# Kernel tuning notes

Hardware: AMD Instinct MI355X
Metric: run time of the kernel (lower is better)

The kernel has to match this reference:

```python
import jax, jax.numpy as jnp
import numpy as np

N = 50000   # nodes
E = 800000  # edges (avg degree 16)
F = 128     # feature dim (input = hidden = output)
H = 8       # heads
D = F // H  # head dim = 16
L = 4       # layers


def setup_inputs() -> dict:
    key = jax.random.key(0)
    ks = jax.random.split(key, 11)
    x = jax.random.normal(ks[0], (N, F), dtype=jnp.float32)
    edge_index = jax.random.randint(ks[1], (2, E), 0, N, dtype=jnp.int64)
    s = 1.0 / np.sqrt(F)
    Wq = jax.random.normal(ks[2], (L, F, F), dtype=jnp.float32) * s
    Wk = jax.random.normal(ks[3], (L, F, F), dtype=jnp.float32) * s
    Wv = jax.random.normal(ks[4], (L, F, F), dtype=jnp.float32) * s
    Ws = jax.random.normal(ks[5], (L, F, F), dtype=jnp.float32) * s  # lin_skip (root weight)
    bq = jax.random.normal(ks[6], (L, F), dtype=jnp.float32) * 0.02
    bk = jax.random.normal(ks[7], (L, F), dtype=jnp.float32) * 0.02
    bv = jax.random.normal(ks[8], (L, F), dtype=jnp.float32) * 0.02
    bs = jax.random.normal(ks[9], (L, F), dtype=jnp.float32) * 0.02
    return {"x": x, "edge_index": edge_index, "Wq": Wq, "bq": bq,
            "Wk": Wk, "bk": bk, "Wv": Wv, "bv": bv, "Ws": Ws, "bs": bs}


def _transformer_conv(x, src, dst, Wq, bq, Wk, bk, Wv, bv, Ws, bs):
    # Q from destination nodes, K/V from source nodes (PyG TransformerConv).
    q = (x @ Wq + bq)[dst].reshape(E, H, D)
    k = (x @ Wk + bk)[src].reshape(E, H, D)
    alpha = (q * k).sum(-1) * (1.0 / np.sqrt(D))            # [E, H]
    # segment softmax over edges grouped by destination node
    amax = jax.ops.segment_max(alpha, dst, num_segments=N)   # [N, H]
    amax = jnp.where(jnp.isfinite(amax), amax, 0.0)
    p = jnp.exp(alpha - amax[dst])
    denom = jax.ops.segment_sum(p, dst, num_segments=N)      # [N, H]
    a = p / denom[dst]                                       # [E, H]
    v = (x @ Wv + bv)[src].reshape(E, H, D)
    msg = (a[..., None] * v).reshape(E, F)
    out = jax.ops.segment_sum(msg, dst, num_segments=N)      # concat heads
    out = out + x @ Ws + bs                                  # root/skip connection
    return out, a


def reference(x, edge_index, Wq, bq, Wk, bk, Wv, bv, Ws, bs):
    src, dst = edge_index[0], edge_index[1]
    alphas = []
    h = x
    for i in range(L - 1):
        h, a = _transformer_conv(h, src, dst, Wq[i], bq[i], Wk[i], bk[i],
                                 Wv[i], bv[i], Ws[i], bs[i])
        h = jax.nn.gelu(h, approximate=False)
        alphas.append(a)
    h, a = _transformer_conv(h, src, dst, Wq[-1], bq[-1], Wk[-1], bk[-1],
                             Wv[-1], bv[-1], Ws[-1], bs[-1])
    alphas.append(a)
    return h, jnp.stack(alphas)  # [N, F], [L, E, H]
```

## Files before the change

### kernel.cpp

```cpp
#include <hip/hip_runtime.h>
#include <math.h>

#define F 128
#define HEADS 8

typedef __attribute__((ext_vector_type(8))) short short8;
typedef __attribute__((ext_vector_type(4))) float floatx4;
typedef __attribute__((ext_vector_type(2))) _Float16 half2v;

__device__ __forceinline__ unsigned short f2bf(float f) {
    unsigned u = __float_as_uint(f);
    unsigned r = u + 0x7FFFu + ((u >> 16) & 1u);
    return (unsigned short)(r >> 16);
}

__device__ __forceinline__ half2v ashalf2(unsigned u) {
    return __builtin_bit_cast(half2v, u);
}
__device__ __forceinline__ unsigned pkh(float a, float b) {
    return __builtin_bit_cast(unsigned, __builtin_amdgcn_cvt_pkrtz(a, b));
}

#if __has_builtin(__builtin_amdgcn_fdot2)
#define FDOT2(a, b, c) __builtin_amdgcn_fdot2((a), (b), (c), false)
#else
#define FDOT2(a, b, c) ((c) + (float)(a)[0] * (float)(b)[0] + (float)(a)[1] * (float)(b)[1])
#endif


__global__ __launch_bounds__(256) void setup_k(
    const float* __restrict__ x, unsigned short* __restrict__ xb, int total4,
    const float* __restrict__ Wq, const float* __restrict__ Wk,
    const float* __restrict__ Wv, const float* __restrict__ Ws,
    unsigned short* __restrict__ wfrag, int wtotal,
    int* __restrict__ deg, int* __restrict__ cursor, int N) {
    int idx = blockIdx.x * 256 + threadIdx.x;
    if (idx < total4) {
        float4 v = ((const float4*)x)[idx];
        ushort4 o;
        o.x = f2bf(v.x); o.y = f2bf(v.y); o.z = f2bf(v.z); o.w = f2bf(v.w);
        ((ushort4*)xb)[idx] = o;
        return;
    }
    idx -= total4;
    if (idx < wtotal) {
        int j = idx & 7;
        int lane = (idx >> 3) & 63;
        int rest = idx >> 9;
        int chunk = rest & 3;
        int ftile = (rest >> 2) & 7;
        int mat = (rest >> 5) & 3;
        int layer = rest >> 7;
        int k = chunk * 32 + (lane >> 4) * 8 + j;
        int f = ftile * 16 + (lane & 15);
        const float* W = (mat == 0) ? Wq : (mat == 1) ? Wk : (mat == 2) ? Wv : Ws;
        wfrag[idx] = f2bf(W[((size_t)layer * F + k) * F + f]);
        return;
    }
    idx -= wtotal;
    if (idx < N) deg[idx] = 0;
    else if (idx < 2 * N) cursor[idx - N] = 0;
}


__global__ __launch_bounds__(256) void hist_k(const int* __restrict__ dst, int E, int* __restrict__ deg) {
    int e = blockIdx.x * 256 + threadIdx.x;
    if (e < E) atomicAdd(&deg[dst[e]], 1);
}

__global__ __launch_bounds__(256) void scan1_k(const int* __restrict__ deg, int N,
                                               int* __restrict__ start, int* __restrict__ partials) {
    __shared__ int sm[256];
    int t = threadIdx.x;
    int i = blockIdx.x * 256 + t;
    int v = (i < N) ? deg[i] : 0;
    sm[t] = v;
    __syncthreads();
    for (int off = 1; off < 256; off <<= 1) {
        int add = (t >= off) ? sm[t - off] : 0;
        __syncthreads();
        sm[t] += add;
        __syncthreads();
    }
    if (i < N) start[i] = sm[t] - v;
    if (t == 255) partials[blockIdx.x] = sm[t];
}

__global__ __launch_bounds__(256) void scan23_k(const int* __restrict__ partials, int nb,
                                                int* __restrict__ start, int N, int E) {
    __shared__ int sm[256];
    int t = threadIdx.x;
    int v = (t < nb) ? partials[t] : 0;
    sm[t] = v;
    __syncthreads();
    for (int off = 1; off < 256; off <<= 1) {
        int add = (t >= off) ? sm[t - off] : 0;
        __syncthreads();
        sm[t] += add;
        __syncthreads();
    }
    int myoff = sm[t] - v;
    __syncthreads();
    sm[t] = myoff;
    __syncthreads();
    for (int i = t; i < N; i += 256) start[i] += sm[i >> 8];
    if (t == 0) start[N] = E;
}

__global__ __launch_bounds__(256) void fill_k(const int* __restrict__ src, const int* __restrict__ dst, int E,
                                              const int* __restrict__ start, int* __restrict__ cursor,
                                              int2* __restrict__ epair) {
    int e = blockIdx.x * 256 + threadIdx.x;
    if (e < E) {
        int dd = dst[e];
        int pos = atomicAdd(&cursor[dd], 1);
        epair[start[dd] + pos] = make_int2(e, src[e]);
    }
}


__global__ __launch_bounds__(256) void gemm_mfma(
    const unsigned short* __restrict__ xb, const unsigned short* __restrict__ wfrag,
    const float* __restrict__ bq, const float* __restrict__ bk,
    const float* __restrict__ bv, const float* __restrict__ bs,
    unsigned short* __restrict__ Qh, unsigned short* __restrict__ Kh,
    unsigned short* __restrict__ Vh, unsigned short* __restrict__ Sh, int N) {
    int wave = threadIdx.x >> 6;
    int lane = threadIdx.x & 63;
    int row0 = blockIdx.x * 32;
    int lm = lane & 15, quad = lane >> 4;
    const unsigned short* wf = wfrag + wave * 16384;

    floatx4 acc[2][8];
#pragma unroll
    for (int t = 0; t < 2; t++)
#pragma unroll
        for (int u = 0; u < 8; u++) acc[t][u] = (floatx4){0.f, 0.f, 0.f, 0.f};

#pragma unroll
    for (int chunk = 0; chunk < 4; chunk++) {
        short8 xfr[2];
#pragma unroll
        for (int t = 0; t < 2; t++) {
            int m = row0 + t * 16 + lm;
            m = (m < N) ? m : (N - 1);
            xfr[t] = *(const short8*)(xb + (size_t)m * F + chunk * 32 + quad * 8);
        }
#pragma unroll
        for (int u = 0; u < 8; u++) {
            short8 wfr = *(const short8*)(wf + ((u * 4 + chunk) * 64 + lane) * 8);
            acc[0][u] = __builtin_amdgcn_mfma_f32_16x16x32_bf16(wfr, xfr[0], acc[0][u], 0, 0, 0);
            acc[1][u] = __builtin_amdgcn_mfma_f32_16x16x32_bf16(wfr, xfr[1], acc[1][u], 0, 0, 0);
        }
    }

    const float* bias = (wave == 0) ? bq : (wave == 1) ? bk : (wave == 2) ? bv : bs;
    unsigned short* dp = (wave == 0) ? Qh : (wave == 1) ? Kh : (wave == 2) ? Vh : Sh;
#pragma unroll
    for (int u = 0; u < 8; u++) {
        float4 bv4 = *(const float4*)&bias[u * 16 + quad * 4];
#pragma unroll
        for (int t = 0; t < 2; t++) {
            int node = row0 + t * 16 + lm;
            if (node < N) {
                floatx4 a = acc[t][u];
                size_t off = (size_t)node * F + u * 16 + quad * 4;
                *(uint2*)&dp[off] = make_uint2(pkh(a[0] + bv4.x, a[1] + bv4.y),
                                               pkh(a[2] + bv4.z, a[3] + bv4.w));
            }
        }
    }
}


__device__ __forceinline__ float gelu_exact(float v) {
    return 0.5f * v * (1.0f + erff(v * 0.70710678118654752f));
}

__global__ __launch_bounds__(256) void edge_k(
    const unsigned short* __restrict__ Qh, const unsigned short* __restrict__ Kh,
    const unsigned short* __restrict__ Vh, const unsigned short* __restrict__ Sh,
    const int* __restrict__ start, const int2* __restrict__ epair,
    float* __restrict__ aout,
    float* __restrict__ hout_f, unsigned short* __restrict__ hout_b,
    int N, int do_gelu) {
    __shared__ float wbuf[4][64][8];
    __shared__ int sbuf[4][64];
    __shared__ int ebuf[4][64];
    __shared__ float mdbuf[4][8];

    int wv = threadIdx.x >> 6;
    int lane = threadIdx.x & 63;
    int n = blockIdx.x * 4 + wv;
    if (n >= N) return;

    int beg = start[n], end = start[n + 1];
    int deg = end - beg;
    bool multi = deg > 64;
    int slot = lane >> 3, h = lane & 7;
    int g = lane >> 4, fl = lane & 15;
    int fh = fl >> 1;

    const unsigned short* qp = Qh + (size_t)n * F + h * 16;
    uint4 qa = *(const uint4*)(qp);
    uint4 qc = *(const uint4*)(qp + 8);
    half2v q0 = ashalf2(qa.x), q1 = ashalf2(qa.y), q2 = ashalf2(qa.z), q3 = ashalf2(qa.w);
    half2v q4 = ashalf2(qc.x), q5 = ashalf2(qc.y), q6 = ashalf2(qc.z), q7 = ashalf2(qc.w);

    float d = 0.f;
    float a0 = 0.f, a1 = 0.f, a2 = 0.f, a3 = 0.f, a4 = 0.f, a5 = 0.f, a6 = 0.f, a7 = 0.f;

    for (int c0 = beg; c0 < end; c0 += 64) {
        int cnt = min(64, end - c0);

        int2 pe = epair[c0 + min(lane, cnt - 1)];
        sbuf[wv][lane] = pe.y << 8;
        ebuf[wv][lane] = pe.x;

        int nit = (cnt + 7) >> 3;
        for (int it = 0; it < nit; it++) {
            int idx = it * 8 + slot;
            bool val = idx < cnt;
            int ofs = sbuf[wv][val ? idx : 0];
            const unsigned short* kp = (const unsigned short*)((const char*)Kh + ofs) + h * 16;
            uint4 ka = *(const uint4*)(kp);
            uint4 kc = *(const uint4*)(kp + 8);
            float p0 = 0.f, p1 = 0.f;
            p0 = FDOT2(q0, ashalf2(ka.x), p0);
            p0 = FDOT2(q1, ashalf2(ka.y), p0);
            p0 = FDOT2(q2, ashalf2(ka.z), p0);
            p0 = FDOT2(q3, ashalf2(ka.w), p0);
            p1 = FDOT2(q4, ashalf2(kc.x), p1);
            p1 = FDOT2(q5, ashalf2(kc.y), p1);
            p1 = FDOT2(q6, ashalf2(kc.z), p1);
            p1 = FDOT2(q7, ashalf2(kc.w), p1);
            float w = __expf((p0 + p1) * 0.25f);
            if (!val) w = 0.f;
            d += w;
            wbuf[wv][idx][h] = w;
            if (multi && val) aout[(size_t)ebuf[wv][idx] * HEADS + h] = w;
        }

        for (int j = 0; j < cnt; j += 8) {
            int idx0 = j + g;
            int idx1 = j + 4 + g;
            bool v0 = idx0 < cnt;
            bool v1 = idx1 < cnt;
            int o0s = sbuf[wv][v0 ? idx0 : 0];
            int o1s = sbuf[wv][v1 ? idx1 : 0];
            float w0 = wbuf[wv][v0 ? idx0 : 0][fh];
            float w1 = wbuf[wv][v1 ? idx1 : 0][fh];
            if (!v0) w0 = 0.f;
            if (!v1) w1 = 0.f;
            uint4 va = *(const uint4*)((const char*)Vh + o0s + fl * 16);
            uint4 vb2 = *(const uint4*)((const char*)Vh + o1s + fl * 16);
            half2v x0 = ashalf2(va.x), x1 = ashalf2(va.y), x2 = ashalf2(va.z), x3 = ashalf2(va.w);
            half2v y0 = ashalf2(vb2.x), y1 = ashalf2(vb2.y), y2 = ashalf2(vb2.z), y3 = ashalf2(vb2.w);
            a0 += w0 * (float)x0[0]; a1 += w0 * (float)x0[1];
            a2 += w0 * (float)x1[0]; a3 += w0 * (float)x1[1];
            a4 += w0 * (float)x2[0]; a5 += w0 * (float)x2[1];
            a6 += w0 * (float)x3[0]; a7 += w0 * (float)x3[1];
            a0 += w1 * (float)y0[0]; a1 += w1 * (float)y0[1];
            a2 += w1 * (float)y1[0]; a3 += w1 * (float)y1[1];
            a4 += w1 * (float)y2[0]; a5 += w1 * (float)y2[1];
            a6 += w1 * (float)y3[0]; a7 += w1 * (float)y3[1];
        }
    }

    d += __shfl_xor(d, 8);
    d += __shfl_xor(d, 16);
    d += __shfl_xor(d, 32);
    float inv_d = (d > 0.f) ? 1.f / d : 0.f;
    if (slot == 0) mdbuf[wv][h] = inv_d;

    if (!multi) {
        for (int idx = slot; idx < deg; idx += 8)
            aout[(size_t)ebuf[wv][idx] * HEADS + h] = wbuf[wv][idx][h] * inv_d;
    } else {
        for (int idx = slot; idx < deg; idx += 8)
            aout[(size_t)epair[beg + idx].x * HEADS + h] *= inv_d;
    }

    *(float4*)&wbuf[wv][lane][0] = make_float4(a0, a1, a2, a3);
    *(float4*)&wbuf[wv][lane][4] = make_float4(a4, a5, a6, a7);
    asm volatile("s_waitcnt lgkmcnt(0)" ::: "memory");

    int f0 = lane * 2;
    int frow = f0 >> 3;
    int fcol = f0 & 7;
    float t0 = 0.f, t1 = 0.f;
#pragma unroll
    for (int gg = 0; gg < 4; gg++) {
        float2 pr = *(const float2*)&wbuf[wv][gg * 16 + frow][fcol];
        t0 += pr.x; t1 += pr.y;
    }
    float invd = mdbuf[wv][lane >> 3];
    half2v s2 = ashalf2(*(const unsigned*)&Sh[(size_t)n * F + f0]);
    float o0 = t0 * invd + (float)s2[0];
    float o1 = t1 * invd + (float)s2[1];
    if (do_gelu) {
        o0 = gelu_exact(o0);
        o1 = gelu_exact(o1);
        unsigned ob = (unsigned)f2bf(o0) | ((unsigned)f2bf(o1) << 16);
        *(unsigned*)&hout_b[(size_t)n * F + f0] = ob;
    } else {
        *(float2*)&hout_f[(size_t)n * F + f0] = make_float2(o0, o1);
    }
}


extern "C" void kernel_launch(void* const* d_in, const int* in_sizes, int n_in,
                              void* d_out, int out_size, void* d_ws, size_t ws_size,
                              hipStream_t stream) {
    const float* x  = (const float*)d_in[0];
    const int*   ei = (const int*)d_in[1];
    const float* Wq = (const float*)d_in[2];
    const float* bq = (const float*)d_in[3];
    const float* Wk = (const float*)d_in[4];
    const float* bk = (const float*)d_in[5];
    const float* Wv = (const float*)d_in[6];
    const float* bv = (const float*)d_in[7];
    const float* Ws = (const float*)d_in[8];
    const float* bs = (const float*)d_in[9];

    const int N = in_sizes[0] / F;
    const int E = in_sizes[1] / 2;
    const int L = in_sizes[2] / (F * F);

    unsigned short* Sh = (unsigned short*)d_ws;
    unsigned short* Qh = Sh + (size_t)N * F;
    unsigned short* xb = Qh + (size_t)N * F;
    unsigned short* hb = xb + (size_t)N * F;
    unsigned short* Kb = hb + (size_t)N * F;
    unsigned short* Vb = Kb + (size_t)N * F;
    unsigned short* wfrag = Vb + (size_t)N * F;
    int2* epair = (int2*)(wfrag + (size_t)L * 4 * 16384);
    int* start = (int*)(epair + E);
    int* cursor = start + (N + 1);
    int* deg = cursor + N;
    int* partials = deg + N;

    float* out_h = (float*)d_out;
    float* out_a = out_h + (size_t)N * F;

    const int* srcIdx = ei;
    const int* dstIdx = ei + E;

    int total4 = N * F / 4;
    int wtotal = L * 4 * 16384;
    int stotal = total4 + wtotal + 2 * N;
    setup_k<<<(stotal + 255) / 256, 256, 0, stream>>>(
        x, xb, total4, Wq, Wk, Wv, Ws, wfrag, wtotal, deg, cursor, N);

    int nbScan = (N + 255) / 256;
    hist_k<<<(E + 255) / 256, 256, 0, stream>>>(dstIdx, E, deg);
    scan1_k<<<nbScan, 256, 0, stream>>>(deg, N, start, partials);
    scan23_k<<<1, 256, 0, stream>>>(partials, nbScan, start, N, E);
    fill_k<<<(E + 255) / 256, 256, 0, stream>>>(srcIdx, dstIdx, E, start, cursor, epair);

    for (int l = 0; l < L; ++l) {
        const unsigned short* hin = (l == 0) ? xb : hb;
        gemm_mfma<<<(N + 31) / 32, 256, 0, stream>>>(
            hin, wfrag + (size_t)l * 4 * 16384,
            bq + (size_t)l * F, bk + (size_t)l * F,
            bv + (size_t)l * F, bs + (size_t)l * F,
            Qh, Kb, Vb, Sh, N);
        edge_k<<<(N + 3) / 4, 256, 0, stream>>>(
            Qh, Kb, Vb, Sh, start, epair,
            out_a + (size_t)l * E * HEADS, out_h, hb, N, (l < L - 1) ? 1 : 0);
    }
}
```

Measured before the change: 668.1 us.

## Interleave K and V rows and fuse V aggregation into score loop

The GEMM now writes K and V into one interleaved buffer, 256 halfs per node, so each edge's source row yields K and V from a single 512-byte region. The edge kernel loads V in the same pass as K and accumulates the unnormalized weighted V per head-slot lane, which removes the separate second gather loop over edges. Per-head sums across the eight slots are done with xor shuffles before normalizing and writing through shared memory. This adds 16 accumulators per lane and 48 shuffles, which raises register pressure, and edge work is no longer spread over the lanes the same way.

```diff
diff --git a/kernel.cpp b/kernel.cpp
--- a/kernel.cpp
+++ b/kernel.cpp
@@ -123,8 +123,8 @@
     const unsigned short* __restrict__ xb, const unsigned short* __restrict__ wfrag,
     const float* __restrict__ bq, const float* __restrict__ bk,
     const float* __restrict__ bv, const float* __restrict__ bs,
-    unsigned short* __restrict__ Qh, unsigned short* __restrict__ Kh,
-    unsigned short* __restrict__ Vh, unsigned short* __restrict__ Sh, int N) {
+    unsigned short* __restrict__ Qh, unsigned short* __restrict__ KV,
+    unsigned short* __restrict__ Sh, int N) {
     int wave = threadIdx.x >> 6;
     int lane = threadIdx.x & 63;
     int row0 = blockIdx.x * 32;
@@ -155,7 +155,10 @@
     }
 
     const float* bias = (wave == 0) ? bq : (wave == 1) ? bk : (wave == 2) ? bv : bs;
-    unsigned short* dp = (wave == 0) ? Qh : (wave == 1) ? Kh : (wave == 2) ? Vh : Sh;
+    unsigned short* dp = (wave == 0) ? Qh : (wave == 3) ? Sh : KV;
+    int kvwave = (wave == 1 || wave == 2);
+    size_t rstride = kvwave ? 256 : 128;
+    size_t roff = (wave == 2) ? 128 : 0;
 #pragma unroll
     for (int u = 0; u < 8; u++) {
         float4 bv4 = *(const float4*)&bias[u * 16 + quad * 4];
@@ -164,7 +167,7 @@
             int node = row0 + t * 16 + lm;
             if (node < N) {
                 floatx4 a = acc[t][u];
-                size_t off = (size_t)node * F + u * 16 + quad * 4;
+                size_t off = (size_t)node * rstride + roff + u * 16 + quad * 4;
                 *(uint2*)&dp[off] = make_uint2(pkh(a[0] + bv4.x, a[1] + bv4.y),
                                                pkh(a[2] + bv4.z, a[3] + bv4.w));
             }
@@ -178,8 +181,8 @@
 }
 
 __global__ __launch_bounds__(256) void edge_k(
-    const unsigned short* __restrict__ Qh, const unsigned short* __restrict__ Kh,
-    const unsigned short* __restrict__ Vh, const unsigned short* __restrict__ Sh,
+    const unsigned short* __restrict__ Qh, const unsigned short* __restrict__ KV,
+    const unsigned short* __restrict__ Sh,
     const int* __restrict__ start, const int2* __restrict__ epair,
     float* __restrict__ aout,
     float* __restrict__ hout_f, unsigned short* __restrict__ hout_b,
@@ -187,7 +190,6 @@
     __shared__ float wbuf[4][64][8];
     __shared__ int sbuf[4][64];
     __shared__ int ebuf[4][64];
-    __shared__ float mdbuf[4][8];
 
     int wv = threadIdx.x >> 6;
     int lane = threadIdx.x & 63;
@@ -198,8 +200,6 @@
     int deg = end - beg;
     bool multi = deg > 64;
     int slot = lane >> 3, h = lane & 7;
-    int g = lane >> 4, fl = lane & 15;
-    int fh = fl >> 1;
 
     const unsigned short* qp = Qh + (size_t)n * F + h * 16;
     uint4 qa = *(const uint4*)(qp);
@@ -208,13 +208,14 @@
     half2v q4 = ashalf2(qc.x), q5 = ashalf2(qc.y), q6 = ashalf2(qc.z), q7 = ashalf2(qc.w);
 
     float d = 0.f;
-    float a0 = 0.f, a1 = 0.f, a2 = 0.f, a3 = 0.f, a4 = 0.f, a5 = 0.f, a6 = 0.f, a7 = 0.f;
+    float b0 = 0.f, b1 = 0.f, b2 = 0.f, b3 = 0.f, b4 = 0.f, b5 = 0.f, b6 = 0.f, b7 = 0.f;
+    float b8 = 0.f, b9 = 0.f, b10 = 0.f, b11 = 0.f, b12 = 0.f, b13 = 0.f, b14 = 0.f, b15 = 0.f;
 
     for (int c0 = beg; c0 < end; c0 += 64) {
         int cnt = min(64, end - c0);
 
         int2 pe = epair[c0 + min(lane, cnt - 1)];
-        sbuf[wv][lane] = pe.y << 8;
+        sbuf[wv][lane] = pe.y << 9;
         ebuf[wv][lane] = pe.x;
 
         int nit = (cnt + 7) >> 3;
@@ -222,9 +223,11 @@
             int idx = it * 8 + slot;
             bool val = idx < cnt;
             int ofs = sbuf[wv][val ? idx : 0];
-            const unsigned short* kp = (const unsigned short*)((const char*)Kh + ofs) + h * 16;
+            const unsigned short* kp = (const unsigned short*)((const char*)KV + ofs) + h * 16;
             uint4 ka = *(const uint4*)(kp);
             uint4 kc = *(const uint4*)(kp + 8);
+            uint4 va = *(const uint4*)(kp + 128);
+            uint4 vc = *(const uint4*)(kp + 136);
             float p0 = 0.f, p1 = 0.f;
             p0 = FDOT2(q0, ashalf2(ka.x), p0);
             p0 = FDOT2(q1, ashalf2(ka.y), p0);
@@ -239,31 +242,16 @@
             d += w;
             wbuf[wv][idx][h] = w;
             if (multi && val) aout[(size_t)ebuf[wv][idx] * HEADS + h] = w;
-        }
-
-        for (int j = 0; j < cnt; j += 8) {
-            int idx0 = j + g;
-            int idx1 = j + 4 + g;
-            bool v0 = idx0 < cnt;
-            bool v1 = idx1 < cnt;
-            int o0s = sbuf[wv][v0 ? idx0 : 0];
-            int o1s = sbuf[wv][v1 ? idx1 : 0];
-            float w0 = wbuf[wv][v0 ? idx0 : 0][fh];
-            float w1 = wbuf[wv][v1 ? idx1 : 0][fh];
-            if (!v0) w0 = 0.f;
-            if (!v1) w1 = 0.f;
-            uint4 va = *(const uint4*)((const char*)Vh + o0s + fl * 16);
-            uint4 vb2 = *(const uint4*)((const char*)Vh + o1s + fl * 16);
             half2v x0 = ashalf2(va.x), x1 = ashalf2(va.y), x2 = ashalf2(va.z), x3 = ashalf2(va.w);
-            half2v y0 = ashalf2(vb2.x), y1 = ashalf2(vb2.y), y2 = ashalf2(vb2.z), y3 = ashalf2(vb2.w);
-            a0 += w0 * (float)x0[0]; a1 += w0 * (float)x0[1];
-            a2 += w0 * (float)x1[0]; a3 += w0 * (float)x1[1];
-            a4 += w0 * (float)x2[0]; a5 += w0 * (float)x2[1];
-            a6 += w0 * (float)x3[0]; a7 += w0 * (float)x3[1];
-            a0 += w1 * (float)y0[0]; a1 += w1 * (float)y0[1];
-            a2 += w1 * (float)y1[0]; a3 += w1 * (float)y1[1];
-            a4 += w1 * (float)y2[0]; a5 += w1 * (float)y2[1];
-            a6 += w1 * (float)y3[0]; a7 += w1 * (float)y3[1];
+            half2v x4 = ashalf2(vc.x), x5 = ashalf2(vc.y), x6 = ashalf2(vc.z), x7 = ashalf2(vc.w);
+            b0  += w * (float)x0[0]; b1  += w * (float)x0[1];
+            b2  += w * (float)x1[0]; b3  += w * (float)x1[1];
+            b4  += w * (float)x2[0]; b5  += w * (float)x2[1];
+            b6  += w * (float)x3[0]; b7  += w * (float)x3[1];
+            b8  += w * (float)x4[0]; b9  += w * (float)x4[1];
+            b10 += w * (float)x5[0]; b11 += w * (float)x5[1];
+            b12 += w * (float)x6[0]; b13 += w * (float)x6[1];
+            b14 += w * (float)x7[0]; b15 += w * (float)x7[1];
         }
     }
 
@@ -271,7 +259,6 @@
     d += __shfl_xor(d, 16);
     d += __shfl_xor(d, 32);
     float inv_d = (d > 0.f) ? 1.f / d : 0.f;
-    if (slot == 0) mdbuf[wv][h] = inv_d;
 
     if (!multi) {
         for (int idx = slot; idx < deg; idx += 8)
@@ -281,23 +268,41 @@
             aout[(size_t)epair[beg + idx].x * HEADS + h] *= inv_d;
     }
 
-    *(float4*)&wbuf[wv][lane][0] = make_float4(a0, a1, a2, a3);
-    *(float4*)&wbuf[wv][lane][4] = make_float4(a4, a5, a6, a7);
+    b0  += __shfl_xor(b0, 8);  b0  += __shfl_xor(b0, 16);  b0  += __shfl_xor(b0, 32);
+    b1  += __shfl_xor(b1, 8);  b1  += __shfl_xor(b1, 16);  b1  += __shfl_xor(b1, 32);
+    b2  += __shfl_xor(b2, 8);  b2  += __shfl_xor(b2, 16);  b2  += __shfl_xor(b2, 32);
+    b3  += __shfl_xor(b3, 8);  b3  += __shfl_xor(b3, 16);  b3  += __shfl_xor(b3, 32);
+    b4  += __shfl_xor(b4, 8);  b4  += __shfl_xor(b4, 16);  b4  += __shfl_xor(b4, 32);
+    b5  += __shfl_xor(b5, 8);  b5  += __shfl_xor(b5, 16);  b5  += __shfl_xor(b5, 32);
+    b6  += __shfl_xor(b6, 8);  b6  += __shfl_xor(b6, 16);  b6  += __shfl_xor(b6, 32);
+    b7  += __shfl_xor(b7, 8);  b7  += __shfl_xor(b7, 16);  b7  += __shfl_xor(b7, 32);
+    b8  += __shfl_xor(b8, 8);  b8  += __shfl_xor(b8, 16);  b8  += __shfl_xor(b8, 32);
+    b9  += __shfl_xor(b9, 8);  b9  += __shfl_xor(b9, 16);  b9  += __shfl_xor(b9, 32);
+    b10 += __shfl_xor(b10, 8); b10 += __shfl_xor(b10, 16); b10 += __shfl_xor(b10, 32);
+    b11 += __shfl_xor(b11, 8); b11 += __shfl_xor(b11, 16); b11 += __shfl_xor(b11, 32);
+    b12 += __shfl_xor(b12, 8); b12 += __shfl_xor(b12, 16); b12 += __shfl_xor(b12, 32);
+    b13 += __shfl_xor(b13, 8); b13 += __shfl_xor(b13, 16); b13 += __shfl_xor(b13, 32);
+    b14 += __shfl_xor(b14, 8); b14 += __shfl_xor(b14, 16); b14 += __shfl_xor(b14, 32);
+    b15 += __shfl_xor(b15, 8); b15 += __shfl_xor(b15, 16); b15 += __shfl_xor(b15, 32);
+
+    float* obuf = &wbuf[wv][0][0];
     asm volatile("s_waitcnt lgkmcnt(0)" ::: "memory");
+    if (slot == 0) {
+        *(float4*)&obuf[h * 16 + 0] = make_float4(b0 * inv_d, b1 * inv_d, b2 * inv_d, b3 * inv_d);
+    } else if (slot == 1) {
+        *(float4*)&obuf[h * 16 + 4] = make_float4(b4 * inv_d, b5 * inv_d, b6 * inv_d, b7 * inv_d);
+    } else if (slot == 2) {
+        *(float4*)&obuf[h * 16 + 8] = make_float4(b8 * inv_d, b9 * inv_d, b10 * inv_d, b11 * inv_d);
+    } else if (slot == 3) {
+        *(float4*)&obuf[h * 16 + 12] = make_float4(b12 * inv_d, b13 * inv_d, b14 * inv_d, b15 * inv_d);
+    }
+    asm volatile("s_waitcnt lgkmcnt(0)" ::: "memory");
 
     int f0 = lane * 2;
-    int frow = f0 >> 3;
-    int fcol = f0 & 7;
-    float t0 = 0.f, t1 = 0.f;
-#pragma unroll
-    for (int gg = 0; gg < 4; gg++) {
-        float2 pr = *(const float2*)&wbuf[wv][gg * 16 + frow][fcol];
-        t0 += pr.x; t1 += pr.y;
-    }
-    float invd = mdbuf[wv][lane >> 3];
+    float2 ov = *(const float2*)&obuf[f0];
     half2v s2 = ashalf2(*(const unsigned*)&Sh[(size_t)n * F + f0]);
-    float o0 = t0 * invd + (float)s2[0];
-    float o1 = t1 * invd + (float)s2[1];
+    float o0 = ov.x + (float)s2[0];
+    float o1 = ov.y + (float)s2[1];
     if (do_gelu) {
         o0 = gelu_exact(o0);
         o1 = gelu_exact(o1);
@@ -331,9 +336,8 @@
     unsigned short* Qh = Sh + (size_t)N * F;
     unsigned short* xb = Qh + (size_t)N * F;
     unsigned short* hb = xb + (size_t)N * F;
-    unsigned short* Kb = hb + (size_t)N * F;
-    unsigned short* Vb = Kb + (size_t)N * F;
-    unsigned short* wfrag = Vb + (size_t)N * F;
+    unsigned short* KV = hb + (size_t)N * F;
+    unsigned short* wfrag = KV + (size_t)N * 2 * F;
     int2* epair = (int2*)(wfrag + (size_t)L * 4 * 16384);
     int* start = (int*)(epair + E);
     int* cursor = start + (N + 1);
@@ -364,9 +368,9 @@
             hin, wfrag + (size_t)l * 4 * 16384,
             bq + (size_t)l * F, bk + (size_t)l * F,
             bv + (size_t)l * F, bs + (size_t)l * F,
-            Qh, Kb, Vb, Sh, N);
+            Qh, KV, Sh, N);
         edge_k<<<(N + 3) / 4, 256, 0, stream>>>(
-            Qh, Kb, Vb, Sh, start, epair,
+            Qh, KV, Sh, start, epair,
             out_a + (size_t)l * E * HEADS, out_h, hb, N, (l < L - 1) ? 1 : 0);
     }
 }
```

Measured after the change: 673.5 us. About the same (+0.8%).
